# Kernel tuning notes

Measured on AMD Instinct MI355X. Metric: run time of the kernel, lower is better.

The kernel has to match this reference:

```python
import jax, jax.numpy as jnp
import numpy as np

N, E, G = 16000, 256000, 64
H, NR, L = 128, 96, 2
CUTOFF = 6.0
EPS = 1e-10

def _ln(x, eps=1e-5):
    m = jnp.mean(x, -1, keepdims=True)
    v = jnp.mean((x - m) ** 2, -1, keepdims=True)
    return (x - m) * jax.lax.rsqrt(v + eps)

def _mlp2(x, w1, b1, w2, b2):
    return jax.nn.silu(x @ w1 + b1) @ w2 + b2

def _xav(key, shape):
    s = (2.0 / (shape[-2] + shape[-1])) ** 0.5
    return jax.random.normal(key, shape, jnp.float32) * s

def setup_inputs():
    key = jax.random.key(0)
    ks = iter(jax.random.split(key, 64))
    pos = jax.random.normal(next(ks), (N, 3), jnp.float32) * 2.0
    z = jax.random.randint(next(ks), (N,), 1, 95)
    batch = jnp.sort(jax.random.randint(next(ks), (N,), 0, G))
    src = jax.random.randint(next(ks), (E,), 0, N)
    off = jax.random.randint(next(ks), (E,), 1, N)
    dst = (src + off) % N  # no self loops -> dist > 0
    edge_index = jnp.stack([src, dst]).astype(jnp.int32)
    H3 = 3 * H
    return dict(
        pos=pos,
        z_emb_w=jax.random.normal(next(ks), (95, H), jnp.float32),
        ne_emb_w=jax.random.normal(next(ks), (95, H), jnp.float32),
        rl_w1=_xav(next(ks), (NR, H)), rl_b1=jnp.zeros((H,), jnp.float32),
        rl_w2=_xav(next(ks), (H, H)), rl_b2=jnp.zeros((H,), jnp.float32),
        sv_w=_xav(next(ks), (H, H)), sv_b=jnp.zeros((H,), jnp.float32),
        lin_w1=_xav(next(ks), (3, H // 4)), lin_b1=jnp.zeros((H // 4,), jnp.float32),
        lin_w2=_xav(next(ks), (H // 4, 1)), lin_b2=jnp.zeros((1,), jnp.float32),
        mp_ln_g=jnp.ones((L, H), jnp.float32), mp_ln_b=jnp.zeros((L, H), jnp.float32),
        mp_xw1=_xav(next(ks), (L, H, H)), mp_xb1=jnp.zeros((L, H), jnp.float32),
        mp_xw2=_xav(next(ks), (L, H, H3)), mp_xb2=jnp.zeros((L, H3), jnp.float32),
        mp_rw=_xav(next(ks), (L, NR, H3)), mp_rb=jnp.zeros((L, H3), jnp.float32),
        mp_dw1=_xav(next(ks), (L, H3 + NR, H3)), mp_db1=jnp.zeros((L, H3), jnp.float32),
        mp_dw2=_xav(next(ks), (L, H3, H3)), mp_db2=jnp.zeros((L, H3), jnp.float32),
        ft_vw=_xav(next(ks), (L, H, 2 * H)),
        ft_xw1=_xav(next(ks), (L, 2 * H, H)), ft_xb1=jnp.zeros((L, H), jnp.float32),
        ft_xw2=_xav(next(ks), (L, H, H3)), ft_xb2=jnp.zeros((L, H3), jnp.float32),
        last_w=_xav(next(ks), (H, 1)), last_b=jnp.zeros((1,), jnp.float32),
        z=z, edge_index=edge_index, batch=batch,
    )

def _forward(pos, z_emb_w, ne_emb_w, rl_w1, rl_b1, rl_w2, rl_b2, sv_w, sv_b,
             lin_w1, lin_b1, lin_w2, lin_b2, mp_ln_g, mp_ln_b, mp_xw1, mp_xb1,
             mp_xw2, mp_xb2, mp_rw, mp_rb, mp_dw1, mp_db1, mp_dw2, mp_db2,
             ft_vw, ft_xw1, ft_xb1, ft_xw2, ft_xb2, last_w, last_b,
             z, edge_index, batch):
    inv_sqrt3 = 1.0 / (3.0 ** 0.5)
    inv_sqrt_h = 1.0 / (H ** 0.5)
    inv_sqrt2 = 1.0 / (2.0 ** 0.5)
    src, dst = edge_index[0], edge_index[1]  # gather from src, scatter-add to dst
    edge_vec = pos[src] - pos[dst]                         # (E,3)
    dist = jnp.sqrt(jnp.sum(edge_vec ** 2, -1))            # (E,)
    # rbf_emb buffers
    start = jnp.exp(jnp.float32(-CUTOFF))
    means = jnp.linspace(start, 1.0, NR)
    betas = (2.0 / NR * (1.0 - start)) ** (-2.0)
    d = dist[:, None]
    rbounds = 0.5 * (jnp.cos(dist * jnp.pi / CUTOFF) + 1.0) * (dist < CUTOFF).astype(dist.dtype)
    rbf = rbounds[:, None] * jnp.exp(-betas * (jnp.exp(-d) - means) ** 2)   # (E,NR)
    rh = rbounds[:, None] * _mlp2(rbf, rl_w1, rl_b1, rl_w2, rl_b2)          # (E,H) radial_hidden
    # embeddings + NeighborEmb (gather-scale-scatter)
    s = _ln(z_emb_w[z])
    sn = _ln(ne_emb_w[z])
    s = s + jax.ops.segment_sum(rh * sn[src], dst, num_segments=N)
    vec = jnp.zeros((N, 3, H), pos.dtype)
    # edge-wise equivariant frame
    edge_diff = edge_vec / d
    edge_cross = jnp.cross(pos[src], pos[dst])
    edge_cross = edge_cross / (jnp.linalg.norm(edge_cross, axis=-1, keepdims=True) + EPS)
    edge_vertical = jnp.cross(edge_diff, edge_cross)
    edge_frame = jnp.stack([edge_diff, edge_cross, edge_vertical], -1)      # (E,3,3)
    # S_vector
    s1 = jax.nn.silu(_ln(s @ sv_w + sv_b))
    msgv = (rh[:, None, :] * edge_diff[:, :, None]) * s1[src][:, None, :]   # (E,3,H)
    S_ij = jax.ops.segment_sum(msgv, dst, num_segments=N)                   # (N,3,H)

    def _scalarize(Sg):
        sc = jnp.einsum('eck,ech->ekh', edge_frame, Sg)    # (E,3,H)
        sc = sc.at[:, 1, :].set(jnp.abs(sc[:, 1, :]))
        p = jnp.transpose(sc, (0, 2, 1))                   # (E,H,3)
        out = _mlp2(p, lin_w1, lin_b1, lin_w2, lin_b2) + p[:, :, 0:1]
        return out[..., 0]                                 # (E,H)

    scalar3 = _scalarize(S_ij[src])
    scalar4 = _scalarize(S_ij[dst])
    edge_weight = jnp.concatenate([scalar3, scalar4], -1) * rbounds[:, None]
    edge_weight = jnp.concatenate([edge_weight, rh, rbf], -1)  # (E, 3H+NR)

    for l in range(L):
        # EquiMessagePassing
        xh = _mlp2(mp_ln_g[l] * _ln(s) + mp_ln_b[l], mp_xw1[l], mp_xb1[l], mp_xw2[l], mp_xb2[l])  # (N,3H)
        rbfh = (rbf @ mp_rw[l] + mp_rb[l]) * _mlp2(edge_weight, mp_dw1[l], mp_db1[l], mp_dw2[l], mp_db2[l])
        m = xh[src] * rbfh                                  # (E,3H)
        mx, m2, m3 = jnp.split(m, 3, -1)
        m2 = m2 * inv_sqrt3
        mvec = (vec[src] * m2[:, None, :] + m3[:, None, :] * edge_diff[:, :, None]) * inv_sqrt_h
        s = (s + jax.ops.segment_sum(mx, dst, num_segments=N)) * inv_sqrt2
        vec = vec + jax.ops.segment_sum(mvec, dst, num_segments=N)
        # FTE (node_frame unused by FTE in the original code)
        vp = jnp.einsum('nch,hk->nck', vec, ft_vw[l])       # (N,3,2H)
        v1, v2 = jnp.split(vp, 2, -1)
        scalar = jnp.sqrt(jnp.sum(v1 ** 2, 1) + 1e-10)      # (N,H)
        vec_dot = jnp.sum(v1 * v2, 1) * inv_sqrt_h
        xvh = _mlp2(jnp.concatenate([s, scalar], -1), ft_xw1[l], ft_xb1[l], ft_xw2[l], ft_xb2[l])
        x1, x2, x3 = jnp.split(xvh, 3, -1)
        s = s + (x1 + x2 + vec_dot) * inv_sqrt2
        vec = vec + x3[:, None, :] * v2

    out = s @ last_w + last_b                               # (N,1)
    return jax.ops.segment_sum(out, batch, num_segments=G)  # (G,1) sum readout

def reference(pos, z_emb_w, ne_emb_w, rl_w1, rl_b1, rl_w2, rl_b2, sv_w, sv_b,
              lin_w1, lin_b1, lin_w2, lin_b2, mp_ln_g, mp_ln_b, mp_xw1, mp_xb1,
              mp_xw2, mp_xb2, mp_rw, mp_rb, mp_dw1, mp_db1, mp_dw2, mp_db2,
              ft_vw, ft_xw1, ft_xb1, ft_xw2, ft_xb2, last_w, last_b,
              z, edge_index, batch):
    return _forward(pos, z_emb_w, ne_emb_w, rl_w1, rl_b1, rl_w2, rl_b2, sv_w, sv_b,
                    lin_w1, lin_b1, lin_w2, lin_b2, mp_ln_g, mp_ln_b, mp_xw1, mp_xb1,
                    mp_xw2, mp_xb2, mp_rw, mp_rb, mp_dw1, mp_db1, mp_dw2, mp_db2,
                    ft_vw, ft_xw1, ft_xb1, ft_xw2, ft_xb2, last_w, last_b,
                    z, edge_index, batch)
```

## Files before the change

### kernel.cpp

```cpp
#include <hip/hip_runtime.h>
#include <math.h>

#define NN 16000
#define NE 256000
#define NG 64
#define HD 128
#define NRAD 96
#define H3 384
#define KD 480

typedef unsigned short u16;
typedef short short8 __attribute__((ext_vector_type(8)));
typedef float f32x4 __attribute__((ext_vector_type(4)));

__device__ __forceinline__ float siluf(float x){ return x / (1.0f + expf(-x)); }

__device__ __forceinline__ float wsum(float v){
#pragma unroll
    for (int o = 32; o > 0; o >>= 1) v += __shfl_xor(v, o, 64);
    return v;
}

__device__ __forceinline__ u16 f2bh(float f){
    unsigned int u = __float_as_uint(f);
    unsigned int r = u + 0x7FFFu + ((u >> 16) & 1u);
    return (u16)(r >> 16);
}
__device__ __forceinline__ float bh2f(u16 h){
    return __uint_as_float((unsigned int)h << 16);
}
__device__ __forceinline__ short8 ld8(const u16* p){ return *(const short8*)p; }

__device__ __forceinline__ void split4(float4 v, uint2& ph, uint2& pl){
    unsigned ux = __float_as_uint(v.x), uy = __float_as_uint(v.y);
    unsigned uz = __float_as_uint(v.z), uw = __float_as_uint(v.w);
    ph.x = __builtin_amdgcn_perm(uy, ux, 0x07060302u);
    ph.y = __builtin_amdgcn_perm(uw, uz, 0x07060302u);
    float lx = v.x - __uint_as_float(ux & 0xFFFF0000u);
    float ly = v.y - __uint_as_float(uy & 0xFFFF0000u);
    float lz = v.z - __uint_as_float(uz & 0xFFFF0000u);
    float lw = v.w - __uint_as_float(uw & 0xFFFF0000u);
    pl.x = __builtin_amdgcn_perm(__float_as_uint(ly), __float_as_uint(lx), 0x07060302u);
    pl.y = __builtin_amdgcn_perm(__float_as_uint(lw), __float_as_uint(lz), 0x07060302u);
}

__global__ void k_fill(float* __restrict__ p, float v, int n){
    int i = blockIdx.x * blockDim.x + threadIdx.x;
    if (i < n) p[i] = v;
}

__global__ void k_wsplit(const float* __restrict__ src, u16* __restrict__ dh, u16* __restrict__ dl,
                         int K, int N){
    int i = blockIdx.x * 256 + threadIdx.x;
    if (i >= K * N) return;
    int n = i / K, k = i - n * K;
    float v = src[(size_t)k * N + n];
    u16 h = f2bh(v);
    dh[i] = h;
    dl[i] = f2bh(v - bh2f(h));
}

__global__ void k_node_embed(const float* __restrict__ zw, const float* __restrict__ nw,
                             const int* __restrict__ z, float* __restrict__ s, float* __restrict__ sn){
    int n = blockIdx.x, t = threadIdx.x;
    int zi = z[n];
    const float* a = zw + (size_t)zi * HD;
    const float* b = nw + (size_t)zi * HD;
    float a0 = a[t], a1 = a[t + 64];
    float m  = wsum(a0 + a1) * (1.f / HD);
    float va = wsum((a0 - m)*(a0 - m) + (a1 - m)*(a1 - m)) * (1.f / HD);
    float r  = rsqrtf(va + 1e-5f);
    s[(size_t)n*HD + t]      = (a0 - m) * r;
    s[(size_t)n*HD + 64 + t] = (a1 - m) * r;
    float b0 = b[t], b1 = b[t + 64];
    m  = wsum(b0 + b1) * (1.f / HD);
    va = wsum((b0 - m)*(b0 - m) + (b1 - m)*(b1 - m)) * (1.f / HD);
    r  = rsqrtf(va + 1e-5f);
    sn[(size_t)n*HD + t]      = (b0 - m) * r;
    sn[(size_t)n*HD + 64 + t] = (b1 - m) * r;
}

__global__ void k_ln_silu(const float* __restrict__ x, float* __restrict__ out){
    int n = blockIdx.x, t = threadIdx.x;
    float a0 = x[(size_t)n*HD + t], a1 = x[(size_t)n*HD + 64 + t];
    float m  = wsum(a0 + a1) * (1.f / HD);
    float va = wsum((a0 - m)*(a0 - m) + (a1 - m)*(a1 - m)) * (1.f / HD);
    float r  = rsqrtf(va + 1e-5f);
    out[(size_t)n*HD + t]      = siluf((a0 - m) * r);
    out[(size_t)n*HD + 64 + t] = siluf((a1 - m) * r);
}

__global__ void k_ln_aff(const float* __restrict__ x, const float* __restrict__ g,
                         const float* __restrict__ b, float* __restrict__ out){
    int n = blockIdx.x, t = threadIdx.x;
    float a0 = x[(size_t)n*HD + t], a1 = x[(size_t)n*HD + 64 + t];
    float m  = wsum(a0 + a1) * (1.f / HD);
    float va = wsum((a0 - m)*(a0 - m) + (a1 - m)*(a1 - m)) * (1.f / HD);
    float r  = rsqrtf(va + 1e-5f);
    out[(size_t)n*HD + t]      = g[t]      * ((a0 - m) * r) + b[t];
    out[(size_t)n*HD + 64 + t] = g[64 + t] * ((a1 - m) * r) + b[64 + t];
}

__global__ void k_edge_geom(const float* __restrict__ pos, const int* __restrict__ ei,
                            float* __restrict__ dist, float* __restrict__ rbnd,
                            float* __restrict__ frame){
    int e = blockIdx.x * blockDim.x + threadIdx.x;
    if (e >= NE) return;
    int si = ei[e], di = ei[NE + e];
    float sx = pos[si*3], sy = pos[si*3+1], sz = pos[si*3+2];
    float dx = pos[di*3], dy = pos[di*3+1], dz = pos[di*3+2];
    float vx = sx - dx, vy = sy - dy, vz = sz - dz;
    float dd = sqrtf(vx*vx + vy*vy + vz*vz);
    dist[e] = dd;
    float rb = (dd < 6.0f) ? 0.5f * (cosf(dd * 0.5235987755982988f) + 1.0f) : 0.0f;
    rbnd[e] = rb;
    float inv = 1.0f / dd;
    float ux = vx*inv, uy = vy*inv, uz = vz*inv;
    float cx = sy*dz - sz*dy, cy = sz*dx - sx*dz, cz = sx*dy - sy*dx;
    float cn = sqrtf(cx*cx + cy*cy + cz*cz) + 1e-10f;
    cx /= cn; cy /= cn; cz /= cn;
    float wx = uy*cz - uz*cy, wy = uz*cx - ux*cz, wz = ux*cy - uy*cx;
    frame[(0*3+0)*NE + e] = ux; frame[(1*3+0)*NE + e] = uy; frame[(2*3+0)*NE + e] = uz;
    frame[(0*3+1)*NE + e] = cx; frame[(1*3+1)*NE + e] = cy; frame[(2*3+1)*NE + e] = cz;
    frame[(0*3+2)*NE + e] = wx; frame[(1*3+2)*NE + e] = wy; frame[(2*3+2)*NE + e] = wz;
}

__global__ void k_rbf(const float* __restrict__ dist, const float* __restrict__ rbnd,
                      float* __restrict__ base, int e0, int ec){
    int idx = blockIdx.x * 256 + threadIdx.x;
    int e = idx / NRAD;
    if (e >= ec) return;
    int k = idx - e * NRAD;
    int eg = e0 + e;
    float start = expf(-6.0f);
    float mean  = start + (1.0f - start) * ((float)k / 95.0f);
    float c     = (2.0f / 96.0f) * (1.0f - start);
    float betas = 1.0f / (c * c);
    float t = expf(-dist[eg]) - mean;
    base[(size_t)e * KD + k] = rbnd[eg] * expf(-betas * t * t);
}

__global__ __launch_bounds__(256)
void mgemm(const float* __restrict__ A, int lda,
           const u16* __restrict__ Bhg, const u16* __restrict__ Blg, int K,
           const float* __restrict__ bias, int act,
           float* __restrict__ C, int ldc,
           int M, int Nn,
           const float* __restrict__ row_scale,
           const float* __restrict__ mulC, int ldm){
    __shared__ u16 Ah[128*40], Al[128*40];
    __shared__ u16 Bh[64*40],  Bl[64*40];
    int tid = threadIdx.x;
    int w = tid >> 6, l = tid & 63;
    int row0 = blockIdx.x * 128, col0 = blockIdx.y * 64;
    f32x4 acc[2][4] = {};
    const int r16 = l & 15, kb = (l >> 4) * 8;

    for (int k0 = 0; k0 < K; k0 += 32){
        if (k0) __syncthreads();
#pragma unroll
        for (int i = 0; i < 4; i++){
            int f = tid + i * 256;
            int r = f >> 3, kq = (f & 7) * 4;
            const float4 v = *(const float4*)(A + (size_t)(row0 + r) * lda + k0 + kq);
            uint2 ph, pl;
            split4(v, ph, pl);
            *(uint2*)&Ah[r*40 + kq] = ph;
            *(uint2*)&Al[r*40 + kq] = pl;
        }
        {
            int bn = tid >> 2, kq = (tid & 3) * 8;
            const size_t gb = (size_t)(col0 + bn) * K + k0 + kq;
            *(short8*)&Bh[bn*40 + kq] = ld8(Bhg + gb);
            *(short8*)&Bl[bn*40 + kq] = ld8(Blg + gb);
        }
        __syncthreads();
        short8 ah0 = *(const short8*)&Ah[(w*32      + r16)*40 + kb];
        short8 ah1 = *(const short8*)&Ah[(w*32 + 16 + r16)*40 + kb];
        short8 al0 = *(const short8*)&Al[(w*32      + r16)*40 + kb];
        short8 al1 = *(const short8*)&Al[(w*32 + 16 + r16)*40 + kb];
#pragma unroll
        for (int nf = 0; nf < 4; nf++){
            short8 bhv = *(const short8*)&Bh[(nf*16 + r16)*40 + kb];
            short8 blv = *(const short8*)&Bl[(nf*16 + r16)*40 + kb];
            acc[0][nf] = __builtin_amdgcn_mfma_f32_16x16x32_bf16(ah0, bhv, acc[0][nf], 0, 0, 0);
            acc[0][nf] = __builtin_amdgcn_mfma_f32_16x16x32_bf16(al0, bhv, acc[0][nf], 0, 0, 0);
            acc[0][nf] = __builtin_amdgcn_mfma_f32_16x16x32_bf16(ah0, blv, acc[0][nf], 0, 0, 0);
            acc[1][nf] = __builtin_amdgcn_mfma_f32_16x16x32_bf16(ah1, bhv, acc[1][nf], 0, 0, 0);
            acc[1][nf] = __builtin_amdgcn_mfma_f32_16x16x32_bf16(al1, bhv, acc[1][nf], 0, 0, 0);
            acc[1][nf] = __builtin_amdgcn_mfma_f32_16x16x32_bf16(ah1, blv, acc[1][nf], 0, 0, 0);
        }
    }
    int rq = (l >> 4) * 4;
#pragma unroll
    for (int mf = 0; mf < 2; mf++){
#pragma unroll
        for (int nf = 0; nf < 4; nf++){
            int n = col0 + nf*16 + r16;
            float bz = bias ? bias[n] : 0.0f;
#pragma unroll
            for (int reg = 0; reg < 4; reg++){
                int m = row0 + w*32 + mf*16 + rq + reg;
                float v = acc[mf][nf][reg] + bz;
                if (act) v = siluf(v);
                if (row_scale) v *= row_scale[m];
                if (mulC) v *= mulC[(size_t)m * ldm + n];
                C[(size_t)m * ldc + n] = v;
            }
        }
    }
}

__global__ __launch_bounds__(256)
void dw2s(const float* __restrict__ hb,
          const float* __restrict__ ewrbf,
          const u16* __restrict__ B1h, const u16* __restrict__ B1l,
          const u16* __restrict__ B2h, const u16* __restrict__ B2l,
          const float* __restrict__ rb, const float* __restrict__ db2,
          const float* __restrict__ xh, const float* __restrict__ vec,
          const float* __restrict__ frame, const int* __restrict__ ei,
          float* __restrict__ s, float* __restrict__ vec_acc, int e0){
    __shared__ u16 Ah[128*40], Al[128*40];
    __shared__ u16 Bh[64*40],  Bl[64*40];
    int tid = threadIdx.x;
    int w = tid >> 6, l = tid & 63;
    int row0 = blockIdx.x * 128, col0 = blockIdx.y * 64;
    const int r16 = l & 15, kb = (l >> 4) * 8;
    f32x4 acc1[2][4] = {}, acc2[2][4] = {};

    for (int k0 = 0; k0 < 96; k0 += 32){
        if (k0) __syncthreads();
#pragma unroll
        for (int i = 0; i < 4; i++){
            int f = tid + i * 256;
            int r = f >> 3, kq = (f & 7) * 4;
            const float4 v = *(const float4*)(ewrbf + (size_t)(row0 + r) * KD + k0 + kq);
            uint2 ph, pl;
            split4(v, ph, pl);
            *(uint2*)&Ah[r*40 + kq] = ph;
            *(uint2*)&Al[r*40 + kq] = pl;
        }
        {
            int bn = tid >> 2, kq = (tid & 3) * 8;
            const size_t gb = (size_t)(col0 + bn) * 96 + k0 + kq;
            *(short8*)&Bh[bn*40 + kq] = ld8(B2h + gb);
            *(short8*)&Bl[bn*40 + kq] = ld8(B2l + gb);
        }
        __syncthreads();
        short8 ah0 = *(const short8*)&Ah[(w*32      + r16)*40 + kb];
        short8 ah1 = *(const short8*)&Ah[(w*32 + 16 + r16)*40 + kb];
        short8 al0 = *(const short8*)&Al[(w*32      + r16)*40 + kb];
        short8 al1 = *(const short8*)&Al[(w*32 + 16 + r16)*40 + kb];
#pragma unroll
        for (int nf = 0; nf < 4; nf++){
            short8 bhv = *(const short8*)&Bh[(nf*16 + r16)*40 + kb];
            short8 blv = *(const short8*)&Bl[(nf*16 + r16)*40 + kb];
            acc2[0][nf] = __builtin_amdgcn_mfma_f32_16x16x32_bf16(ah0, bhv, acc2[0][nf], 0, 0, 0);
            acc2[0][nf] = __builtin_amdgcn_mfma_f32_16x16x32_bf16(al0, bhv, acc2[0][nf], 0, 0, 0);
            acc2[0][nf] = __builtin_amdgcn_mfma_f32_16x16x32_bf16(ah0, blv, acc2[0][nf], 0, 0, 0);
            acc2[1][nf] = __builtin_amdgcn_mfma_f32_16x16x32_bf16(ah1, bhv, acc2[1][nf], 0, 0, 0);
            acc2[1][nf] = __builtin_amdgcn_mfma_f32_16x16x32_bf16(al1, bhv, acc2[1][nf], 0, 0, 0);
            acc2[1][nf] = __builtin_amdgcn_mfma_f32_16x16x32_bf16(ah1, blv, acc2[1][nf], 0, 0, 0);
        }
    }
    for (int k0 = 0; k0 < H3; k0 += 32){
        __syncthreads();
#pragma unroll
        for (int i = 0; i < 4; i++){
            int f = tid + i * 256;
            int r = f >> 3, kq = (f & 7) * 4;
            const float4 v = *(const float4*)(hb + (size_t)(row0 + r) * H3 + k0 + kq);
            uint2 ph, pl;
            split4(v, ph, pl);
            *(uint2*)&Ah[r*40 + kq] = ph;
            *(uint2*)&Al[r*40 + kq] = pl;
        }
        {
            int bn = tid >> 2, kq = (tid & 3) * 8;
            const size_t gb = (size_t)(col0 + bn) * H3 + k0 + kq;
            *(short8*)&Bh[bn*40 + kq] = ld8(B1h + gb);
            *(short8*)&Bl[bn*40 + kq] = ld8(B1l + gb);
        }
        __syncthreads();
        short8 ah0 = *(const short8*)&Ah[(w*32      + r16)*40 + kb];
        short8 ah1 = *(const short8*)&Ah[(w*32 + 16 + r16)*40 + kb];
        short8 al0 = *(const short8*)&Al[(w*32      + r16)*40 + kb];
        short8 al1 = *(const short8*)&Al[(w*32 + 16 + r16)*40 + kb];
#pragma unroll
        for (int nf = 0; nf < 4; nf++){
            short8 bhv = *(const short8*)&Bh[(nf*16 + r16)*40 + kb];
            short8 blv = *(const short8*)&Bl[(nf*16 + r16)*40 + kb];
            acc1[0][nf] = __builtin_amdgcn_mfma_f32_16x16x32_bf16(ah0, bhv, acc1[0][nf], 0, 0, 0);
            acc1[0][nf] = __builtin_amdgcn_mfma_f32_16x16x32_bf16(al0, bhv, acc1[0][nf], 0, 0, 0);
            acc1[0][nf] = __builtin_amdgcn_mfma_f32_16x16x32_bf16(ah0, blv, acc1[0][nf], 0, 0, 0);
            acc1[1][nf] = __builtin_amdgcn_mfma_f32_16x16x32_bf16(ah1, bhv, acc1[1][nf], 0, 0, 0);
            acc1[1][nf] = __builtin_amdgcn_mfma_f32_16x16x32_bf16(al1, bhv, acc1[1][nf], 0, 0, 0);
            acc1[1][nf] = __builtin_amdgcn_mfma_f32_16x16x32_bf16(ah1, blv, acc1[1][nf], 0, 0, 0);
        }
    }
    int rq = (l >> 4) * 4;
    int br = col0 >> 7;
    int ho = col0 & 127;
#pragma unroll
    for (int mf = 0; mf < 2; mf++){
#pragma unroll
        for (int reg = 0; reg < 4; reg++){
            int m  = row0 + w*32 + mf*16 + rq + reg;
            int eg = e0 + m;
            int si = ei[eg], di = ei[NE + eg];
            float df0 = 0.f, df1 = 0.f, df2 = 0.f;
            if (br == 2){
                df0 = frame[0*NE + eg];
                df1 = frame[3*NE + eg];
                df2 = frame[6*NE + eg];
            }
#pragma unroll
            for (int nf = 0; nf < 4; nf++){
                int n = col0 + nf*16 + r16;
                int h = ho + nf*16 + r16;
                float v  = (acc2[mf][nf][reg] + rb[n]) * (acc1[mf][nf][reg] + db2[n]);
                float xv = xh[(size_t)si * H3 + n];
                if (br == 0){
                    atomicAdd(&s[(size_t)di * HD + h], xv * v);
                } else if (br == 1){
                    float m2 = xv * v * 0.5773502691896258f;
                    size_t sb = (size_t)si * H3, db = (size_t)di * H3;
#pragma unroll
                    for (int c = 0; c < 3; c++)
                        atomicAdd(&vec_acc[db + c*HD + h],
                                  vec[sb + c*HD + h] * m2 * 0.08838834764831845f);
                } else {
                    float m3 = xv * v * 0.08838834764831845f;
                    size_t db = (size_t)di * H3;
                    atomicAdd(&vec_acc[db + 0*HD + h], m3 * df0);
                    atomicAdd(&vec_acc[db + 1*HD + h], m3 * df1);
                    atomicAdd(&vec_acc[db + 2*HD + h], m3 * df2);
                }
            }
        }
    }
}

struct WT { u16* h; u16* l; };

static void gemm(hipStream_t st, const float* A, int lda, WT B,
                 const float* bias, float* C, int ldc, size_t M, int K, int Nn,
                 int act, const float* rs, const float* mul, int ldm){
    dim3 g((unsigned)(M / 128), (unsigned)(Nn / 64)), b(256);
    mgemm<<<g, b, 0, st>>>(A, lda, B.h, B.l, K, bias, act, C, ldc, (int)M, Nn, rs, mul, ldm);
}

__global__ void k_scatter_s(const float* __restrict__ rh, const float* __restrict__ sn,
                            const int* __restrict__ ei, float* __restrict__ s, int e0, int ec){
    int idx = blockIdx.x * 256 + threadIdx.x;
    int e = idx >> 7, h = idx & 127;
    if (e >= ec) return;
    int eg = e0 + e;
    int si = ei[eg], di = ei[NE + eg];
    atomicAdd(&s[(size_t)di * HD + h], rh[(size_t)e * KD + h] * sn[(size_t)si * HD + h]);
}

__global__ void k_scatter_msgv(const float* __restrict__ rh, const float* __restrict__ s1,
                               const float* __restrict__ frame, const int* __restrict__ ei,
                               float* __restrict__ S_ij, int e0, int ec){
    int idx = blockIdx.x * 256 + threadIdx.x;
    int e = idx >> 7, h = idx & 127;
    if (e >= ec) return;
    int eg = e0 + e;
    int si = ei[eg], di = ei[NE + eg];
    float mv = rh[(size_t)e * KD + h] * s1[(size_t)si * HD + h];
    size_t db = (size_t)di * H3;
#pragma unroll
    for (int c = 0; c < 3; c++){
        float df = frame[(c*3 + 0) * NE + eg];
        atomicAdd(&S_ij[db + c * HD + h], mv * df);
    }
}

__global__ void k_scalarize(const float* __restrict__ S_ij, const float* __restrict__ frame,
                            const float* __restrict__ rbnd, const int* __restrict__ ei,
                            const float* __restrict__ w1, const float* __restrict__ b1,
                            const float* __restrict__ w2, const float* __restrict__ b2v,
                            float* __restrict__ base, int e0){
    int e = blockIdx.x, h = threadIdx.x;
    int eg = e0 + e;
    int si = ei[eg], di = ei[NE + eg];
    float fr[9];
#pragma unroll
    for (int i = 0; i < 9; i++) fr[i] = frame[i * NE + eg];
    float rb = rbnd[eg];
    float b2 = b2v[0];
#pragma unroll
    for (int g = 0; g < 2; g++){
        int node = g ? di : si;
        float S0 = S_ij[(size_t)node * H3 + h];
        float S1 = S_ij[(size_t)node * H3 + 128 + h];
        float S2 = S_ij[(size_t)node * H3 + 256 + h];
        float p0 = fr[0]*S0 + fr[3]*S1 + fr[6]*S2;
        float p1 = fabsf(fr[1]*S0 + fr[4]*S1 + fr[7]*S2);
        float p2 = fr[2]*S0 + fr[5]*S1 + fr[8]*S2;
        float o = b2 + p0;
#pragma unroll
        for (int j = 0; j < 32; j++){
            float hh = siluf(p0 * w1[j] + p1 * w1[32 + j] + p2 * w1[64 + j] + b1[j]);
            o += hh * w2[j];
        }
        base[(size_t)e * KD + g * 128 + h] = o * rb;
    }
}

__global__ void k_scale_s(float* __restrict__ s){
    int i = blockIdx.x * 256 + threadIdx.x;
    s[i] *= 0.7071067811865476f;
}

__global__ void k_vec_add(float* __restrict__ vec, const float* __restrict__ vec_acc){
    int i = blockIdx.x * 256 + threadIdx.x;
    vec[i] += vec_acc[i];
}

__global__ void k_vfeat(const float* __restrict__ vp, const float* __restrict__ s,
                        float* __restrict__ t256, float* __restrict__ vdot){
    int idx = blockIdx.x * 256 + threadIdx.x;
    int n = idx >> 7, h = idx & 127;
    float a = 0.f, b = 0.f;
#pragma unroll
    for (int c = 0; c < 3; c++){
        float v1 = vp[(size_t)(n*3 + c) * 256 + h];
        float v2 = vp[(size_t)(n*3 + c) * 256 + 128 + h];
        a += v1 * v1;
        b += v1 * v2;
    }
    t256[(size_t)n * 256 + 128 + h] = sqrtf(a + 1e-10f);
    vdot[idx] = b * 0.08838834764831845f;
    t256[(size_t)n * 256 + h] = s[idx];
}

__global__ void k_upd_s(float* __restrict__ s, const float* __restrict__ xvh,
                        const float* __restrict__ vdot){
    int idx = blockIdx.x * 256 + threadIdx.x;
    int n = idx >> 7, h = idx & 127;
    s[idx] += (xvh[(size_t)n * H3 + h] + xvh[(size_t)n * H3 + 128 + h] + vdot[idx]) * 0.7071067811865476f;
}

__global__ void k_upd_vec(float* __restrict__ vec, const float* __restrict__ xvh,
                          const float* __restrict__ vp){
    int idx = blockIdx.x * 256 + threadIdx.x;
    int n = idx / H3;
    int r = idx - n * H3;
    int c = r >> 7, h = r & 127;
    vec[idx] += xvh[(size_t)n * H3 + 256 + h] * vp[(size_t)(n*3 + c) * 256 + 128 + h];
}

__global__ void k_final(const float* __restrict__ s, const float* __restrict__ lw,
                        const float* __restrict__ lb, const int* __restrict__ batch,
                        float* __restrict__ out){
    int n = blockIdx.x, t = threadIdx.x;
    float v = s[(size_t)n * HD + t] * lw[t] + s[(size_t)n * HD + 64 + t] * lw[64 + t];
    v = wsum(v);
    if (t == 0) atomicAdd(&out[batch[n]], v + lb[0]);
}

extern "C" void kernel_launch(void* const* d_in, const int* in_sizes, int n_in,
                              void* d_out, int out_size, void* d_ws, size_t ws_size,
                              hipStream_t stream){
    const float* pos      = (const float*)d_in[0];
    const float* z_emb_w  = (const float*)d_in[1];
    const float* ne_emb_w = (const float*)d_in[2];
    const float* rl_w1    = (const float*)d_in[3];
    const float* rl_b1    = (const float*)d_in[4];
    const float* rl_w2    = (const float*)d_in[5];
    const float* rl_b2    = (const float*)d_in[6];
    const float* sv_w     = (const float*)d_in[7];
    const float* sv_b     = (const float*)d_in[8];
    const float* lin_w1   = (const float*)d_in[9];
    const float* lin_b1   = (const float*)d_in[10];
    const float* lin_w2   = (const float*)d_in[11];
    const float* lin_b2   = (const float*)d_in[12];
    const float* mp_ln_g  = (const float*)d_in[13];
    const float* mp_ln_b  = (const float*)d_in[14];
    const float* mp_xw1   = (const float*)d_in[15];
    const float* mp_xb1   = (const float*)d_in[16];
    const float* mp_xw2   = (const float*)d_in[17];
    const float* mp_xb2   = (const float*)d_in[18];
    const float* mp_rw    = (const float*)d_in[19];
    const float* mp_rb    = (const float*)d_in[20];
    const float* mp_dw1   = (const float*)d_in[21];
    const float* mp_db1   = (const float*)d_in[22];
    const float* mp_dw2   = (const float*)d_in[23];
    const float* mp_db2   = (const float*)d_in[24];
    const float* ft_vw    = (const float*)d_in[25];
    const float* ft_xw1   = (const float*)d_in[26];
    const float* ft_xb1   = (const float*)d_in[27];
    const float* ft_xw2   = (const float*)d_in[28];
    const float* ft_xb2   = (const float*)d_in[29];
    const float* last_w   = (const float*)d_in[30];
    const float* last_b   = (const float*)d_in[31];
    const int*   z        = (const int*)d_in[32];
    const int*   ei       = (const int*)d_in[33];
    const int*   batch    = (const int*)d_in[34];
    float* out = (float*)d_out;
    (void)in_sizes; (void)n_in; (void)out_size;

    float* ws = (float*)d_ws;
    size_t off = 0;
    auto alloc = [&](size_t nf){ float* p = ws + off; off += (nf + 63) & ~(size_t)63; return p; };

    float* s       = alloc((size_t)NN * HD);
    float* sn      = alloc((size_t)NN * HD);
    float* s1      = alloc((size_t)NN * HD);
    float* tA      = alloc((size_t)NN * HD);
    float* vdot    = alloc((size_t)NN * HD);
    float* vec     = alloc((size_t)NN * H3);
    float* vec_acc = alloc((size_t)NN * H3);
    float* S_ij    = alloc((size_t)NN * H3);
    float* xh      = alloc((size_t)NN * H3);
    float* vp      = alloc((size_t)NN * 3 * 256);
    float* dist    = alloc((size_t)NE);
    float* rbnd    = alloc((size_t)NE);
    float* frame   = alloc((size_t)NE * 9);
    float* t256    = sn;

    const size_t WELEMS = 45056 + 2 * 548864;
    u16* wcur = (u16*)alloc(WELEMS);
    auto wsplit = [&](const float* src, int K, int N)->WT{
        WT r; r.h = wcur; wcur += (size_t)K * N; r.l = wcur; wcur += (size_t)K * N;
        k_wsplit<<<(unsigned)(((size_t)K * N + 255) / 256), 256, 0, stream>>>(src, r.h, r.l, K, N);
        return r;
    };
    WT W_rl1 = wsplit(rl_w1, NRAD, HD);
    WT W_rl2 = wsplit(rl_w2, HD, HD);
    WT W_sv  = wsplit(sv_w, HD, HD);
    WT W_xw1[2], W_xw2[2], W_rw[2], W_dw1[2], W_dw2[2], W_vw[2], W_fx1[2], W_fx2[2];
    for (int l = 0; l < 2; l++){
        W_xw1[l] = wsplit(mp_xw1 + (size_t)l * HD * HD, HD, HD);
        W_xw2[l] = wsplit(mp_xw2 + (size_t)l * HD * H3, HD, H3);
        W_rw[l]  = wsplit(mp_rw  + (size_t)l * NRAD * H3, NRAD, H3);
        W_dw1[l] = wsplit(mp_dw1 + (size_t)l * KD * H3, KD, H3);
        W_dw2[l] = wsplit(mp_dw2 + (size_t)l * H3 * H3, H3, H3);
        W_vw[l]  = wsplit(ft_vw  + (size_t)l * HD * 256, HD, 256);
        W_fx1[l] = wsplit(ft_xw1 + (size_t)l * 256 * HD, 256, HD);
        W_fx2[l] = wsplit(ft_xw2 + (size_t)l * HD * H3, HD, H3);
    }

    size_t availF = ws_size / sizeof(float);
    size_t rem = (availF > off + 1024) ? (availF - off - 1024) : 0;
    const size_t EWF = (size_t)NE * KD;
    bool persist;
    size_t CE;
    float* ew  = nullptr;
    float* ewc = nullptr;
    if (rem >= EWF + 128 * 384 + 256){
        persist = true;
        ew = alloc(EWF);
        rem = availF - off - 1024;
        size_t ce = rem / (size_t)H3;
        CE = ce & ~(size_t)127;
        if (CE < 128) CE = 128;
        if (CE > NE) CE = NE;
    } else {
        persist = false;
        size_t ce = rem / ((size_t)KD + (size_t)H3);
        CE = ce & ~(size_t)127;
        if (CE < 128) CE = 128;
        if (CE > NE) CE = NE;
        ewc = alloc(CE * KD);
    }
    float* hbuf = alloc(CE * (size_t)H3);

    auto build_rh = [&](size_t e0, size_t ec, float* base){
        k_rbf<<<(unsigned)((ec * NRAD) / 256), 256, 0, stream>>>(dist, rbnd, base + 384, (int)e0, (int)ec);
        gemm(stream, base + 384, KD, W_rl1, rl_b1, hbuf, HD, ec, NRAD, HD, 1, nullptr, nullptr, 0);
        gemm(stream, hbuf, HD, W_rl2, rl_b2, base + 256, KD, ec, HD, HD, 0, rbnd + e0, nullptr, 0);
    };

    k_fill<<<1, 64, 0, stream>>>(out, 0.f, NG);
    k_node_embed<<<NN, 64, 0, stream>>>(z_emb_w, ne_emb_w, z, s, sn);
    k_edge_geom<<<NE / 256, 256, 0, stream>>>(pos, ei, dist, rbnd, frame);

    for (size_t e0 = 0; e0 < NE; e0 += CE){
        size_t ec = (NE - e0 < CE) ? (NE - e0) : CE;
        float* base = persist ? (ew + e0 * KD) : ewc;
        build_rh(e0, ec, base);
        k_scatter_s<<<(unsigned)((ec * HD) / 256), 256, 0, stream>>>(base + 256, sn, ei, s, (int)e0, (int)ec);
    }

    gemm(stream, s, HD, W_sv, sv_b, tA, HD, NN, HD, HD, 0, nullptr, nullptr, 0);
    k_ln_silu<<<NN, 64, 0, stream>>>(tA, s1);

    k_fill<<<(NN * H3) / 256, 256, 0, stream>>>(S_ij, 0.f, NN * H3);
    for (size_t e0 = 0; e0 < NE; e0 += CE){
        size_t ec = (NE - e0 < CE) ? (NE - e0) : CE;
        float* base = persist ? (ew + e0 * KD) : ewc;
        if (!persist) build_rh(e0, ec, base);
        k_scatter_msgv<<<(unsigned)((ec * HD) / 256), 256, 0, stream>>>(base + 256, s1, frame, ei, S_ij, (int)e0, (int)ec);
    }

    if (persist)
        k_scalarize<<<NE, 128, 0, stream>>>(S_ij, frame, rbnd, ei, lin_w1, lin_b1, lin_w2, lin_b2, ew, 0);

    k_fill<<<(NN * H3) / 256, 256, 0, stream>>>(vec, 0.f, NN * H3);

    for (int l = 0; l < 2; l++){
        k_ln_aff<<<NN, 64, 0, stream>>>(s, mp_ln_g + l * HD, mp_ln_b + l * HD, tA);
        gemm(stream, tA, HD, W_xw1[l], mp_xb1 + l * HD, vdot, HD, NN, HD, HD, 1, nullptr, nullptr, 0);
        gemm(stream, vdot, HD, W_xw2[l], mp_xb2 + l * H3, xh, H3, NN, HD, H3, 0, nullptr, nullptr, 0);

        k_fill<<<(NN * H3) / 256, 256, 0, stream>>>(vec_acc, 0.f, NN * H3);

        for (size_t e0 = 0; e0 < NE; e0 += CE){
            size_t ec = (NE - e0 < CE) ? (NE - e0) : CE;
            float* base = persist ? (ew + e0 * KD) : ewc;
            if (!persist){
                build_rh(e0, ec, base);
                k_scalarize<<<(unsigned)ec, 128, 0, stream>>>(S_ij, frame, rbnd, ei, lin_w1, lin_b1, lin_w2, lin_b2, base, (int)e0);
            }
            gemm(stream, base, KD, W_dw1[l], mp_db1 + l * H3, hbuf, H3, ec, KD, H3, 1, nullptr, nullptr, 0);
            dim3 g((unsigned)(ec / 128), 6);
            dw2s<<<g, 256, 0, stream>>>(hbuf, base + 384,
                                        W_dw2[l].h, W_dw2[l].l, W_rw[l].h, W_rw[l].l,
                                        mp_rb + l * H3, mp_db2 + l * H3,
                                        xh, vec, frame, ei, s, vec_acc, (int)e0);
        }
        k_scale_s<<<(NN * HD) / 256, 256, 0, stream>>>(s);
        k_vec_add<<<(NN * H3) / 256, 256, 0, stream>>>(vec, vec_acc);

        gemm(stream, vec, HD, W_vw[l], nullptr, vp, 256, (size_t)NN * 3, HD, 256, 0, nullptr, nullptr, 0);
        k_vfeat<<<(NN * HD) / 256, 256, 0, stream>>>(vp, s, t256, vdot);

        gemm(stream, t256, 256, W_fx1[l], ft_xb1 + l * HD, tA, HD, NN, 256, HD, 1, nullptr, nullptr, 0);
        gemm(stream, tA, HD, W_fx2[l], ft_xb2 + l * H3, xh, H3, NN, HD, H3, 0, nullptr, nullptr, 0);

        k_upd_s<<<(NN * HD) / 256, 256, 0, stream>>>(s, xh, vdot);
        k_upd_vec<<<(NN * H3) / 256, 256, 0, stream>>>(vec, xh, vp);
    }

    k_final<<<NN, 64, 0, stream>>>(s, last_w, last_b, batch, out);
}
```

Before: 10.63 ms.

## Split edge message kernel and merge vector branches to halve vec_acc atomics

Splits the fused edge-message epilogue kernel into a scalar-branch kernel that scatters into s and a vector kernel that computes the two vector branches (columns 128-255 and 256-383) together in one block. Each block then sums both contributions before issuing three atomics per element into vec_acc instead of six. This is meant to cut global atomic traffic and redundant index/xh loads. In exchange the vector kernel holds twice the accumulators and twice the B tile in shared memory, which raises register and LDS pressure and may lower occupancy. It also adds an extra kernel launch per edge chunk.

```diff
diff --git a/kernel.cpp b/kernel.cpp
--- a/kernel.cpp
+++ b/kernel.cpp
@@ -212,14 +212,13 @@
 }
 
 __global__ __launch_bounds__(256)
-void dw2s(const float* __restrict__ hb,
-          const float* __restrict__ ewrbf,
-          const u16* __restrict__ B1h, const u16* __restrict__ B1l,
-          const u16* __restrict__ B2h, const u16* __restrict__ B2l,
-          const float* __restrict__ rb, const float* __restrict__ db2,
-          const float* __restrict__ xh, const float* __restrict__ vec,
-          const float* __restrict__ frame, const int* __restrict__ ei,
-          float* __restrict__ s, float* __restrict__ vec_acc, int e0){
+void dw2s_mx(const float* __restrict__ hb,
+             const float* __restrict__ ewrbf,
+             const u16* __restrict__ B1h, const u16* __restrict__ B1l,
+             const u16* __restrict__ B2h, const u16* __restrict__ B2l,
+             const float* __restrict__ rb, const float* __restrict__ db2,
+             const float* __restrict__ xh, const int* __restrict__ ei,
+             float* __restrict__ s, int e0){
     __shared__ u16 Ah[128*40], Al[128*40];
     __shared__ u16 Bh[64*40],  Bl[64*40];
     int tid = threadIdx.x;
@@ -299,8 +298,6 @@
         }
     }
     int rq = (l >> 4) * 4;
-    int br = col0 >> 7;
-    int ho = col0 & 127;
 #pragma unroll
     for (int mf = 0; mf < 2; mf++){
 #pragma unroll
@@ -308,34 +305,152 @@
             int m  = row0 + w*32 + mf*16 + rq + reg;
             int eg = e0 + m;
             int si = ei[eg], di = ei[NE + eg];
-            float df0 = 0.f, df1 = 0.f, df2 = 0.f;
-            if (br == 2){
-                df0 = frame[0*NE + eg];
-                df1 = frame[3*NE + eg];
-                df2 = frame[6*NE + eg];
-            }
 #pragma unroll
             for (int nf = 0; nf < 4; nf++){
                 int n = col0 + nf*16 + r16;
-                int h = ho + nf*16 + r16;
                 float v  = (acc2[mf][nf][reg] + rb[n]) * (acc1[mf][nf][reg] + db2[n]);
                 float xv = xh[(size_t)si * H3 + n];
-                if (br == 0){
-                    atomicAdd(&s[(size_t)di * HD + h], xv * v);
-                } else if (br == 1){
-                    float m2 = xv * v * 0.5773502691896258f;
-                    size_t sb = (size_t)si * H3, db = (size_t)di * H3;
-#pragma unroll
-                    for (int c = 0; c < 3; c++)
-                        atomicAdd(&vec_acc[db + c*HD + h],
-                                  vec[sb + c*HD + h] * m2 * 0.08838834764831845f);
-                } else {
-                    float m3 = xv * v * 0.08838834764831845f;
-                    size_t db = (size_t)di * H3;
-                    atomicAdd(&vec_acc[db + 0*HD + h], m3 * df0);
-                    atomicAdd(&vec_acc[db + 1*HD + h], m3 * df1);
-                    atomicAdd(&vec_acc[db + 2*HD + h], m3 * df2);
-                }
+                atomicAdd(&s[(size_t)di * HD + n], xv * v);
+            }
+        }
+    }
+}
+
+__global__ __launch_bounds__(256)
+void dw2s_vec(const float* __restrict__ hb,
+              const float* __restrict__ ewrbf,
+              const u16* __restrict__ B1h, const u16* __restrict__ B1l,
+              const u16* __restrict__ B2h, const u16* __restrict__ B2l,
+              const float* __restrict__ rb, const float* __restrict__ db2,
+              const float* __restrict__ xh, const float* __restrict__ vec,
+              const float* __restrict__ frame, const int* __restrict__ ei,
+              float* __restrict__ vec_acc, int e0){
+    __shared__ u16 Ah[128*40], Al[128*40];
+    __shared__ u16 Bh[128*40], Bl[128*40];
+    int tid = threadIdx.x;
+    int w = tid >> 6, l = tid & 63;
+    int row0 = blockIdx.x * 128;
+    int ho = blockIdx.y * 64;
+    int n1b = 128 + ho, n2b = 256 + ho;
+    const int r16 = l & 15, kb = (l >> 4) * 8;
+    f32x4 a1a[2][4] = {}, a2a[2][4] = {};
+    f32x4 a1b[2][4] = {}, a2b[2][4] = {};
+
+    for (int k0 = 0; k0 < 96; k0 += 32){
+        if (k0) __syncthreads();
+#pragma unroll
+        for (int i = 0; i < 4; i++){
+            int f = tid + i * 256;
+            int r = f >> 3, kq = (f & 7) * 4;
+            const float4 v = *(const float4*)(ewrbf + (size_t)(row0 + r) * KD + k0 + kq);
+            uint2 ph, pl;
+            split4(v, ph, pl);
+            *(uint2*)&Ah[r*40 + kq] = ph;
+            *(uint2*)&Al[r*40 + kq] = pl;
+        }
+        {
+            int bn = tid >> 1, kq = (tid & 1) * 16;
+            int col = (bn < 64) ? (n1b + bn) : (n2b + bn - 64);
+            const size_t gb = (size_t)col * 96 + k0 + kq;
+            *(short8*)&Bh[bn*40 + kq]     = ld8(B2h + gb);
+            *(short8*)&Bh[bn*40 + kq + 8] = ld8(B2h + gb + 8);
+            *(short8*)&Bl[bn*40 + kq]     = ld8(B2l + gb);
+            *(short8*)&Bl[bn*40 + kq + 8] = ld8(B2l + gb + 8);
+        }
+        __syncthreads();
+        short8 ah0 = *(const short8*)&Ah[(w*32      + r16)*40 + kb];
+        short8 ah1 = *(const short8*)&Ah[(w*32 + 16 + r16)*40 + kb];
+        short8 al0 = *(const short8*)&Al[(w*32      + r16)*40 + kb];
+        short8 al1 = *(const short8*)&Al[(w*32 + 16 + r16)*40 + kb];
+#pragma unroll
+        for (int nf = 0; nf < 4; nf++){
+            short8 bhv = *(const short8*)&Bh[(nf*16 + r16)*40 + kb];
+            short8 blv = *(const short8*)&Bl[(nf*16 + r16)*40 + kb];
+            a2a[0][nf] = __builtin_amdgcn_mfma_f32_16x16x32_bf16(ah0, bhv, a2a[0][nf], 0, 0, 0);
+            a2a[0][nf] = __builtin_amdgcn_mfma_f32_16x16x32_bf16(al0, bhv, a2a[0][nf], 0, 0, 0);
+            a2a[0][nf] = __builtin_amdgcn_mfma_f32_16x16x32_bf16(ah0, blv, a2a[0][nf], 0, 0, 0);
+            a2a[1][nf] = __builtin_amdgcn_mfma_f32_16x16x32_bf16(ah1, bhv, a2a[1][nf], 0, 0, 0);
+            a2a[1][nf] = __builtin_amdgcn_mfma_f32_16x16x32_bf16(al1, bhv, a2a[1][nf], 0, 0, 0);
+            a2a[1][nf] = __builtin_amdgcn_mfma_f32_16x16x32_bf16(ah1, blv, a2a[1][nf], 0, 0, 0);
+            short8 bhw = *(const short8*)&Bh[(64 + nf*16 + r16)*40 + kb];
+            short8 blw = *(const short8*)&Bl[(64 + nf*16 + r16)*40 + kb];
+            a2b[0][nf] = __builtin_amdgcn_mfma_f32_16x16x32_bf16(ah0, bhw, a2b[0][nf], 0, 0, 0);
+            a2b[0][nf] = __builtin_amdgcn_mfma_f32_16x16x32_bf16(al0, bhw, a2b[0][nf], 0, 0, 0);
+            a2b[0][nf] = __builtin_amdgcn_mfma_f32_16x16x32_bf16(ah0, blw, a2b[0][nf], 0, 0, 0);
+            a2b[1][nf] = __builtin_amdgcn_mfma_f32_16x16x32_bf16(ah1, bhw, a2b[1][nf], 0, 0, 0);
+            a2b[1][nf] = __builtin_amdgcn_mfma_f32_16x16x32_bf16(al1, bhw, a2b[1][nf], 0, 0, 0);
+            a2b[1][nf] = __builtin_amdgcn_mfma_f32_16x16x32_bf16(ah1, blw, a2b[1][nf], 0, 0, 0);
+        }
+    }
+    for (int k0 = 0; k0 < H3; k0 += 32){
+        __syncthreads();
+#pragma unroll
+        for (int i = 0; i < 4; i++){
+            int f = tid + i * 256;
+            int r = f >> 3, kq = (f & 7) * 4;
+            const float4 v = *(const float4*)(hb + (size_t)(row0 + r) * H3 + k0 + kq);
+            uint2 ph, pl;
+            split4(v, ph, pl);
+            *(uint2*)&Ah[r*40 + kq] = ph;
+            *(uint2*)&Al[r*40 + kq] = pl;
+        }
+        {
+            int bn = tid >> 1, kq = (tid & 1) * 16;
+            int col = (bn < 64) ? (n1b + bn) : (n2b + bn - 64);
+            const size_t gb = (size_t)col * H3 + k0 + kq;
+            *(short8*)&Bh[bn*40 + kq]     = ld8(B1h + gb);
+            *(short8*)&Bh[bn*40 + kq + 8] = ld8(B1h + gb + 8);
+            *(short8*)&Bl[bn*40 + kq]     = ld8(B1l + gb);
+            *(short8*)&Bl[bn*40 + kq + 8] = ld8(B1l + gb + 8);
+        }
+        __syncthreads();
+        short8 ah0 = *(const short8*)&Ah[(w*32      + r16)*40 + kb];
+        short8 ah1 = *(const short8*)&Ah[(w*32 + 16 + r16)*40 + kb];
+        short8 al0 = *(const short8*)&Al[(w*32      + r16)*40 + kb];
+        short8 al1 = *(const short8*)&Al[(w*32 + 16 + r16)*40 + kb];
+#pragma unroll
+        for (int nf = 0; nf < 4; nf++){
+            short8 bhv = *(const short8*)&Bh[(nf*16 + r16)*40 + kb];
+            short8 blv = *(const short8*)&Bl[(nf*16 + r16)*40 + kb];
+            a1a[0][nf] = __builtin_amdgcn_mfma_f32_16x16x32_bf16(ah0, bhv, a1a[0][nf], 0, 0, 0);
+            a1a[0][nf] = __builtin_amdgcn_mfma_f32_16x16x32_bf16(al0, bhv, a1a[0][nf], 0, 0, 0);
+            a1a[0][nf] = __builtin_amdgcn_mfma_f32_16x16x32_bf16(ah0, blv, a1a[0][nf], 0, 0, 0);
+            a1a[1][nf] = __builtin_amdgcn_mfma_f32_16x16x32_bf16(ah1, bhv, a1a[1][nf], 0, 0, 0);
+            a1a[1][nf] = __builtin_amdgcn_mfma_f32_16x16x32_bf16(al1, bhv, a1a[1][nf], 0, 0, 0);
+            a1a[1][nf] = __builtin_amdgcn_mfma_f32_16x16x32_bf16(ah1, blv, a1a[1][nf], 0, 0, 0);
+            short8 bhw = *(const short8*)&Bh[(64 + nf*16 + r16)*40 + kb];
+            short8 blw = *(const short8*)&Bl[(64 + nf*16 + r16)*40 + kb];
+            a1b[0][nf] = __builtin_amdgcn_mfma_f32_16x16x32_bf16(ah0, bhw, a1b[0][nf], 0, 0, 0);
+            a1b[0][nf] = __builtin_amdgcn_mfma_f32_16x16x32_bf16(al0, bhw, a1b[0][nf], 0, 0, 0);
+            a1b[0][nf] = __builtin_amdgcn_mfma_f32_16x16x32_bf16(ah0, blw, a1b[0][nf], 0, 0, 0);
+            a1b[1][nf] = __builtin_amdgcn_mfma_f32_16x16x32_bf16(ah1, bhw, a1b[1][nf], 0, 0, 0);
+            a1b[1][nf] = __builtin_amdgcn_mfma_f32_16x16x32_bf16(al1, bhw, a1b[1][nf], 0, 0, 0);
+            a1b[1][nf] = __builtin_amdgcn_mfma_f32_16x16x32_bf16(ah1, blw, a1b[1][nf], 0, 0, 0);
+        }
+    }
+    int rq = (l >> 4) * 4;
+#pragma unroll
+    for (int mf = 0; mf < 2; mf++){
+#pragma unroll
+        for (int reg = 0; reg < 4; reg++){
+            int m  = row0 + w*32 + mf*16 + rq + reg;
+            int eg = e0 + m;
+            int si = ei[eg], di = ei[NE + eg];
+            float df0 = frame[0*NE + eg];
+            float df1 = frame[3*NE + eg];
+            float df2 = frame[6*NE + eg];
+            size_t sb = (size_t)si * H3, db = (size_t)di * H3;
+#pragma unroll
+            for (int nf = 0; nf < 4; nf++){
+                int h  = ho + nf*16 + r16;
+                int n1 = 128 + h, n2 = 256 + h;
+                float va = (a2a[mf][nf][reg] + rb[n1]) * (a1a[mf][nf][reg] + db2[n1]);
+                float vb = (a2b[mf][nf][reg] + rb[n2]) * (a1b[mf][nf][reg] + db2[n2]);
+                float m2 = xh[sb + n1] * va * 0.5773502691896258f * 0.08838834764831845f;
+                float m3 = xh[sb + n2] * vb * 0.08838834764831845f;
+                atomicAdd(&vec_acc[db + 0*HD + h], vec[sb + 0*HD + h] * m2 + m3 * df0);
+                atomicAdd(&vec_acc[db + 1*HD + h], vec[sb + 1*HD + h] * m2 + m3 * df1);
+                atomicAdd(&vec_acc[db + 2*HD + h], vec[sb + 2*HD + h] * m2 + m3 * df2);
             }
         }
     }
@@ -616,11 +731,16 @@
                 k_scalarize<<<(unsigned)ec, 128, 0, stream>>>(S_ij, frame, rbnd, ei, lin_w1, lin_b1, lin_w2, lin_b2, base, (int)e0);
             }
             gemm(stream, base, KD, W_dw1[l], mp_db1 + l * H3, hbuf, H3, ec, KD, H3, 1, nullptr, nullptr, 0);
-            dim3 g((unsigned)(ec / 128), 6);
-            dw2s<<<g, 256, 0, stream>>>(hbuf, base + 384,
-                                        W_dw2[l].h, W_dw2[l].l, W_rw[l].h, W_rw[l].l,
-                                        mp_rb + l * H3, mp_db2 + l * H3,
-                                        xh, vec, frame, ei, s, vec_acc, (int)e0);
+            dim3 gm((unsigned)(ec / 128), 2);
+            dw2s_mx<<<gm, 256, 0, stream>>>(hbuf, base + 384,
+                                            W_dw2[l].h, W_dw2[l].l, W_rw[l].h, W_rw[l].l,
+                                            mp_rb + l * H3, mp_db2 + l * H3,
+                                            xh, ei, s, (int)e0);
+            dim3 gv((unsigned)(ec / 128), 2);
+            dw2s_vec<<<gv, 256, 0, stream>>>(hbuf, base + 384,
+                                             W_dw2[l].h, W_dw2[l].l, W_rw[l].h, W_rw[l].l,
+                                             mp_rb + l * H3, mp_db2 + l * H3,
+                                             xh, vec, frame, ei, vec_acc, (int)e0);
         }
         k_scale_s<<<(NN * HD) / 256, 256, 0, stream>>>(s);
         k_vec_add<<<(NN * H3) / 256, 256, 0, stream>>>(vec, vec_acc);
```

After: 12.05 ms. 13.4% more time.
